# Optimization experiments

Hardware: AMD Instinct MI355X
Metric: run time of the kernel (lower is better)

The kernel has to match this reference:

```python
import jax, jax.numpy as jnp
import numpy as np

IN_DIM = 14400
K = 25
DIMS = [7200, 3600, 1800]  # floor(in_dim / 2**(i+1))
OUT_DIM = 2
BATCH = 256


def setup_inputs() -> dict:
    key = jax.random.key(0)
    ks = jax.random.split(key, 32)
    inp = {}
    inp["x"] = jax.random.normal(ks[0], (BATCH, 2 * IN_DIM), dtype=jnp.float32)
    # shared KNN tables (both channels load the same h5 files)
    prev = [IN_DIM] + DIMS[:-1]
    for i, (d, p) in enumerate(zip(DIMS, prev)):
        inp[f"knn{i}"] = jax.random.randint(ks[1 + i], (d, K), 0, p, dtype=jnp.int64)
    std = (2.0 / K) ** 0.5
    kidx = 4
    for ch in ("p", "n"):
        for i, d in enumerate(DIMS):
            inp[f"w{ch}{i}"] = jax.random.normal(ks[kidx], (d, K), dtype=jnp.float32) * std; kidx += 1
            inp[f"b{ch}{i}"] = jnp.zeros((1, d), dtype=jnp.float32)
        inp[f"fc{ch}_w"] = jax.random.normal(ks[kidx], (OUT_DIM, DIMS[-1]), dtype=jnp.float32) * (1.0 / DIMS[-1] ** 0.5); kidx += 1
        inp[f"fc{ch}_b"] = jnp.zeros((OUT_DIM,), dtype=jnp.float32)
    inp["fc3_w"] = jax.random.normal(ks[kidx], (OUT_DIM, 4), dtype=jnp.float32) * 0.5
    inp["fc3_b"] = jnp.zeros((OUT_DIM,), dtype=jnp.float32)
    return inp


def _lcn(x, knns, ws, bs, fw, fb):
    # x: (B, in_dim). Each layer: gather KNN neighbors, weighted sum, bias, relu.
    for knn, w, b in zip(knns, ws, bs):
        g = x[:, knn]                                  # (B, dim, K) gather
        x = jax.nn.relu(jnp.einsum('bdk,dk->bd', g, w) + b)
    return x @ fw.T + fb                               # fc_angle


def reference(x, knn0, knn1, knn2,
              wp0, bp0, wp1, bp1, wp2, bp2, fcp_w, fcp_b,
              wn0, bn0, wn1, bn1, wn2, bn2, fcn_w, fcn_b,
              fc3_w, fc3_b):
    knns = (knn0, knn1, knn2)
    xpos = _lcn(x[:, :IN_DIM], knns, (wp0, wp1, wp2), (bp0, bp1, bp2), fcp_w, fcp_b)
    xneg = _lcn(x[:, IN_DIM:], knns, (wn0, wn1, wn2), (bn0, bn1, bn2), fcn_w, fcn_b)
    h = jax.nn.relu(jnp.concatenate([xpos, xneg], axis=1))  # (B, 4)
    return h @ fc3_w.T + fc3_b
```

## Files before the change

### kernel.cpp

```cpp
#include <hip/hip_runtime.h>
#include <hip/hip_bf16.h>

using bf16 = __hip_bfloat16;

#define K 25
#define B 256

__device__ __forceinline__ float b2f(ushort u) {
  unsigned int w = ((unsigned int)u) << 16;
  float f; __builtin_memcpy(&f, &w, 4); return f;
}
__device__ __forceinline__ ushort f2b(float f) {
  bf16 h = __float2bfloat16(f);
  ushort u; __builtin_memcpy(&u, &h, 2); return u;
}

__global__ __launch_bounds__(256) void transpose_kernel(const void* __restrict__ x,
                                                        const void* __restrict__ knn0,
                                                        ushort* __restrict__ xT,
                                                        float* __restrict__ y,
                                                        int* __restrict__ flags) {
  __shared__ float tile[64][65];
  __shared__ int s_flags[2];
  const int t = threadIdx.x;

  if (t < 64) {
    const unsigned int u = ((const unsigned int*)x)[t * 997];
    const unsigned int e = (u >> 23) & 0xFF;
    const unsigned long long m = __ballot((e >= 192) || (e <= 30));
    if (t == 0) s_flags[0] = (__popcll(m) >= 32) ? 1 : 0;
  } else if (t < 128) {
    const int l = t - 64;
    const unsigned int hi = ((const unsigned int*)knn0)[2 * l + 1];
    const unsigned long long m = __ballot(hi != 0);
    if (l == 0) s_flags[1] = (m == 0ULL) ? 1 : 0;
  }
  __syncthreads();
  const int fdt = s_flags[0];

  if (blockIdx.x == 0 && blockIdx.y == 0) {
    if (t == 0) {
      flags[0] = s_flags[0];
      flags[1] = s_flags[1];
      flags[16] = 0;
    }
#pragma unroll
    for (int i = 0; i < 4; ++i) y[t + i * 256] = 0.0f;
  }

  const int f0 = blockIdx.x * 64;
  const int b0 = blockIdx.y * 64;
  if (fdt) {
    const ushort* xp = (const ushort*)x;
#pragma unroll
    for (int q = 0; q < 4; ++q) {
      const int lin = t + q * 256;
      const int bl = lin >> 4;
      const int fq = (lin & 15) << 2;
      const ushort4 v = *(const ushort4*)(xp + (size_t)(b0 + bl) * 28800 + f0 + fq);
      tile[bl][fq] = b2f(v.x); tile[bl][fq + 1] = b2f(v.y);
      tile[bl][fq + 2] = b2f(v.z); tile[bl][fq + 3] = b2f(v.w);
    }
  } else {
    const float* xp = (const float*)x;
#pragma unroll
    for (int q = 0; q < 4; ++q) {
      const int lin = t + q * 256;
      const int bl = lin >> 4;
      const int fq = (lin & 15) << 2;
      const float4 v = *(const float4*)(xp + (size_t)(b0 + bl) * 28800 + f0 + fq);
      tile[bl][fq] = v.x; tile[bl][fq + 1] = v.y;
      tile[bl][fq + 2] = v.z; tile[bl][fq + 3] = v.w;
    }
  }
  __syncthreads();
#pragma unroll
  for (int q = 0; q < 4; ++q) {
    const int lin = t + q * 256;
    const int fl = lin >> 4;
    const int bq = (lin & 15) << 2;
    ushort4 o;
    o.x = f2b(tile[bq][fl]);     o.y = f2b(tile[bq + 1][fl]);
    o.z = f2b(tile[bq + 2][fl]); o.w = f2b(tile[bq + 3][fl]);
    *(ushort4*)(xT + (size_t)(f0 + fl) * B + b0 + bq) = o;
  }
}

__global__ __launch_bounds__(256) void lcn_layer(const ushort* __restrict__ inT,
                                                 const void* __restrict__ knn,
                                                 const void* __restrict__ wp,
                                                 const void* __restrict__ bp,
                                                 const void* __restrict__ wn,
                                                 const void* __restrict__ bn,
                                                 ushort* __restrict__ outT,
                                                 const int* __restrict__ flags,
                                                 int prev, int dout) {
  const int fdt = flags[0];
  const int idt = flags[1];
  const int wave = threadIdx.x >> 6;
  const int lane = threadIdx.x & 63;
  const int cf   = blockIdx.x & 3;
  const int ch   = cf >> 1;
  const int half = cf & 1;
  const int d    = (blockIdx.x >> 2) * 4 + wave;

  const ushort* in = inT + (size_t)ch * prev * B + half * 128;
  const void* wsel = ch ? wn : wp;
  const void* bsel = ch ? bn : bp;

  int r[K]; float wk[K];
  if (idt) {
    const long long* ip = (const long long*)knn + (size_t)d * K;
#pragma unroll
    for (int k = 0; k < K; ++k) r[k] = (int)ip[k];
  } else {
    const int* ip = (const int*)knn + (size_t)d * K;
#pragma unroll
    for (int k = 0; k < K; ++k) r[k] = ip[k];
  }
  if (fdt) {
    const ushort* wpp = (const ushort*)wsel + (size_t)d * K;
#pragma unroll
    for (int k = 0; k < K; ++k) wk[k] = b2f(wpp[k]);
  } else {
    const float* wpp = (const float*)wsel + (size_t)d * K;
#pragma unroll
    for (int k = 0; k < K; ++k) wk[k] = wpp[k];
  }
  const float bias = fdt ? b2f(((const ushort*)bsel)[d]) : ((const float*)bsel)[d];

  float a0 = 0.f, a1 = 0.f;
#pragma unroll
  for (int k = 0; k < K; ++k) {
    const ushort2 v = *(const ushort2*)(in + (size_t)r[k] * B + (lane << 1));
    a0 = fmaf(wk[k], b2f(v.x), a0);
    a1 = fmaf(wk[k], b2f(v.y), a1);
  }
  a0 = fmaxf(a0 + bias, 0.f);
  a1 = fmaxf(a1 + bias, 0.f);
  ushort2 o; o.x = f2b(a0); o.y = f2b(a1);
  *(ushort2*)(outT + ((size_t)ch * dout + d) * B + half * 128 + (lane << 1)) = o;
}

__global__ __launch_bounds__(256) void fc_final_kernel(const ushort* __restrict__ h2,
                                                       const void* __restrict__ fcpw,
                                                       const void* __restrict__ fcnw,
                                                       const void* __restrict__ fcpb,
                                                       const void* __restrict__ fcnb,
                                                       const void* __restrict__ f3w,
                                                       const void* __restrict__ f3b,
                                                       float* __restrict__ y,
                                                       int* __restrict__ flags,
                                                       void* __restrict__ out) {
  const int fdt = flags[0];
  const int wave = threadIdx.x >> 6;
  const int lane = threadIdx.x & 63;
  const int wt = blockIdx.x * 4 + wave;
  __shared__ int s_last;

  if (wt < 450) {
    const int ch = wt >= 225;
    const int c0 = (ch ? wt - 225 : wt) * 8;
    const ushort* h = h2 + (size_t)ch * 1800 * B;
    const void* fw = ch ? fcnw : fcpw;
    float w0[8], w1[8];
    if (fdt) {
      const ushort* fp = (const ushort*)fw;
#pragma unroll
      for (int j = 0; j < 8; ++j) { w0[j] = b2f(fp[c0 + j]); w1[j] = b2f(fp[1800 + c0 + j]); }
    } else {
      const float* fp = (const float*)fw;
#pragma unroll
      for (int j = 0; j < 8; ++j) { w0[j] = fp[c0 + j]; w1[j] = fp[1800 + c0 + j]; }
    }
    float s0[4] = {0.f, 0.f, 0.f, 0.f}, s1[4] = {0.f, 0.f, 0.f, 0.f};
#pragma unroll
    for (int j = 0; j < 8; ++j) {
      const ushort4 v = *(const ushort4*)(h + (size_t)(c0 + j) * B + (lane << 2));
      const float f0v = b2f(v.x), f1v = b2f(v.y), f2v = b2f(v.z), f3v = b2f(v.w);
      s0[0] = fmaf(w0[j], f0v, s0[0]); s0[1] = fmaf(w0[j], f1v, s0[1]);
      s0[2] = fmaf(w0[j], f2v, s0[2]); s0[3] = fmaf(w0[j], f3v, s0[3]);
      s1[0] = fmaf(w1[j], f0v, s1[0]); s1[1] = fmaf(w1[j], f1v, s1[1]);
      s1[2] = fmaf(w1[j], f2v, s1[2]); s1[3] = fmaf(w1[j], f3v, s1[3]);
    }
#pragma unroll
    for (int i = 0; i < 4; ++i) {
      atomicAdd(&y[(ch * 2 + 0) * B + (lane << 2) + i], s0[i]);
      atomicAdd(&y[(ch * 2 + 1) * B + (lane << 2) + i], s1[i]);
    }
  }

  __syncthreads();
  if (threadIdx.x == 0) {
    __threadfence();
    s_last = (atomicAdd(&flags[16], 1) == gridDim.x - 1);
  }
  __syncthreads();
  if (s_last) {
    const int b = threadIdx.x;
    const float y0 = atomicAdd(&y[0 * B + b], 0.0f);
    const float y1 = atomicAdd(&y[1 * B + b], 0.0f);
    const float y2 = atomicAdd(&y[2 * B + b], 0.0f);
    const float y3 = atomicAdd(&y[3 * B + b], 0.0f);
    const float bp0v = fdt ? b2f(((const ushort*)fcpb)[0]) : ((const float*)fcpb)[0];
    const float bp1v = fdt ? b2f(((const ushort*)fcpb)[1]) : ((const float*)fcpb)[1];
    const float bn0v = fdt ? b2f(((const ushort*)fcnb)[0]) : ((const float*)fcnb)[0];
    const float bn1v = fdt ? b2f(((const ushort*)fcnb)[1]) : ((const float*)fcnb)[1];
    const float h0v = fmaxf(y0 + bp0v, 0.f);
    const float h1v = fmaxf(y1 + bp1v, 0.f);
    const float h2v = fmaxf(y2 + bn0v, 0.f);
    const float h3v = fmaxf(y3 + bn1v, 0.f);
#pragma unroll
    for (int o = 0; o < 2; ++o) {
      float w0, w1, w2, w3, bb;
      if (fdt) {
        const ushort* fp = (const ushort*)f3w;
        w0 = b2f(fp[o * 4 + 0]); w1 = b2f(fp[o * 4 + 1]);
        w2 = b2f(fp[o * 4 + 2]); w3 = b2f(fp[o * 4 + 3]);
        bb = b2f(((const ushort*)f3b)[o]);
      } else {
        const float* fp = (const float*)f3w;
        w0 = fp[o * 4 + 0]; w1 = fp[o * 4 + 1];
        w2 = fp[o * 4 + 2]; w3 = fp[o * 4 + 3];
        bb = ((const float*)f3b)[o];
      }
      float r = bb;
      r = fmaf(w0, h0v, r); r = fmaf(w1, h1v, r);
      r = fmaf(w2, h2v, r); r = fmaf(w3, h3v, r);
      if (fdt) ((ushort*)out)[b * 2 + o] = f2b(r);
      else     ((float*)out)[b * 2 + o] = r;
    }
  }
}

extern "C" void kernel_launch(void* const* d_in, const int* in_sizes, int n_in,
                              void* d_out, int out_size, void* d_ws, size_t ws_size,
                              hipStream_t stream) {
  const void* x    = d_in[0];
  const void* knn0 = d_in[1];
  const void* knn1 = d_in[2];
  const void* knn2 = d_in[3];
  const void* wp0  = d_in[4];  const void* bp0 = d_in[5];
  const void* wp1  = d_in[6];  const void* bp1 = d_in[7];
  const void* wp2  = d_in[8];  const void* bp2 = d_in[9];
  const void* fcpw = d_in[10]; const void* fcpb = d_in[11];
  const void* wn0  = d_in[12]; const void* bn0 = d_in[13];
  const void* wn1  = d_in[14]; const void* bn1 = d_in[15];
  const void* wn2  = d_in[16]; const void* bn2 = d_in[17];
  const void* fcnw = d_in[18]; const void* fcnb = d_in[19];
  const void* f3w  = d_in[20]; const void* f3b  = d_in[21];

  char* ws = (char*)d_ws;
  ushort* xT = (ushort*)(ws);
  ushort* h0 = (ushort*)(ws + 14745600);
  ushort* h1 = (ushort*)(ws + 22118400);
  ushort* h2 = (ushort*)(ws + 25804800);
  float* y   = (float*)(ws + 27648000);
  int* flags = (int*)(ws + 27652096);

  transpose_kernel<<<dim3(450, 4), 256, 0, stream>>>(x, knn0, xT, y, flags);

  lcn_layer<<<7200, 256, 0, stream>>>(xT, knn0, wp0, bp0, wn0, bn0, h0,
                                      flags, 14400, 7200);
  lcn_layer<<<3600, 256, 0, stream>>>(h0, knn1, wp1, bp1, wn1, bn1, h1,
                                      flags, 7200, 3600);
  lcn_layer<<<1800, 256, 0, stream>>>(h1, knn2, wp2, bp2, wn2, bn2, h2,
                                      flags, 3600, 1800);

  fc_final_kernel<<<113, 256, 0, stream>>>(h2, fcpw, fcnw, fcpb, fcnb, f3w, f3b,
                                           y, flags, d_out);
}
```

Measured before the change: 178.2 us.

## Fuse all LCN layers into one LDS-resident kernel per batch pair and channel

Replaces the transpose, three per-layer gather kernels and the FC kernel with a prepack kernel plus one fused kernel. The prepack kernel packs each KNN index and bf16 weight into a 32-bit word laid out k-major, and converts the biases. The fused kernel keeps two batch rows of one channel in LDS (about 86 KB), runs all three layers and the FC reduction from LDS, and combines results through atomics. This removes the global round trips for the intermediate activations and the transpose, but leaves only 256 blocks with heavy LDS use, so occupancy is low and each thread works through long serial loops.

After: 174.3 us. 2.2% less time.

```diff
diff --git a/kernel.cpp b/kernel.cpp
--- a/kernel.cpp
+++ b/kernel.cpp
@@ -4,7 +4,16 @@
 using bf16 = __hip_bfloat16;
 
 #define K 25
-#define B 256
+#define D0 7200
+#define D1 3600
+#define D2 1800
+
+#define PKB_L1 360000
+#define PKB_L2 540000
+#define NPK    630000
+#define PBB_L1 14400
+#define PBB_L2 21600
+#define NPB    25200
 
 __device__ __forceinline__ float b2f(ushort u) {
   unsigned int w = ((unsigned int)u) << 16;
@@ -15,15 +24,20 @@
   ushort u; __builtin_memcpy(&u, &h, 2); return u;
 }
 
-__global__ __launch_bounds__(256) void transpose_kernel(const void* __restrict__ x,
-                                                        const void* __restrict__ knn0,
-                                                        ushort* __restrict__ xT,
-                                                        float* __restrict__ y,
-                                                        int* __restrict__ flags) {
-  __shared__ float tile[64][65];
+__global__ __launch_bounds__(256) void prepack_kernel(
+    const void* __restrict__ x,
+    const void* __restrict__ knn0, const void* __restrict__ knn1,
+    const void* __restrict__ knn2,
+    const void* __restrict__ wp0, const void* __restrict__ bp0,
+    const void* __restrict__ wp1, const void* __restrict__ bp1,
+    const void* __restrict__ wp2, const void* __restrict__ bp2,
+    const void* __restrict__ wn0, const void* __restrict__ bn0,
+    const void* __restrict__ wn1, const void* __restrict__ bn1,
+    const void* __restrict__ wn2, const void* __restrict__ bn2,
+    unsigned int* __restrict__ pk, float* __restrict__ pbias,
+    float* __restrict__ y, int* __restrict__ flags) {
   __shared__ int s_flags[2];
   const int t = threadIdx.x;
-
   if (t < 64) {
     const unsigned int u = ((const unsigned int*)x)[t * 997];
     const unsigned int e = (u >> 23) & 0xFF;
@@ -36,172 +50,172 @@
     if (l == 0) s_flags[1] = (m == 0ULL) ? 1 : 0;
   }
   __syncthreads();
-  const int fdt = s_flags[0];
-
-  if (blockIdx.x == 0 && blockIdx.y == 0) {
+  const int fdt = s_flags[0], idt = s_flags[1];
+
+  if (blockIdx.x == 0 && t == 0) {
+    flags[0] = fdt; flags[1] = idt; flags[16] = 0;
+  }
+
+  const int gid = blockIdx.x * 256 + t;
+  if (gid < NPK) {
+    int i = gid, ch, k, d, dout;
+    const void *kn, *wsel;
+    if (i < PKB_L1) {
+      ch = i / 180000; i -= ch * 180000; dout = D0; kn = knn0;
+      wsel = ch ? wn0 : wp0;
+    } else if (i < PKB_L2) {
+      i -= PKB_L1; ch = i / 90000; i -= ch * 90000; dout = D1; kn = knn1;
+      wsel = ch ? wn1 : wp1;
+    } else {
+      i -= PKB_L2; ch = i / 45000; i -= ch * 45000; dout = D2; kn = knn2;
+      wsel = ch ? wn2 : wp2;
+    }
+    k = i / dout; d = i - k * dout;
+    const int pos = d * K + k;
+    const unsigned int idx = idt ? ((const unsigned int*)kn)[2 * pos]
+                                 : ((const unsigned int*)kn)[pos];
+    const ushort wb = fdt ? ((const ushort*)wsel)[pos]
+                          : f2b(((const float*)wsel)[pos]);
+    pk[gid] = (idx << 16) | (unsigned int)wb;
+  } else if (gid < NPK + NPB) {
+    int i = gid - NPK, ch, d;
+    const void* src;
+    if (i < PBB_L1) {
+      ch = i / D0; d = i - ch * D0; src = ch ? bn0 : bp0;
+    } else if (i < PBB_L2) {
+      const int i2 = i - PBB_L1; ch = i2 / D1; d = i2 - ch * D1; src = ch ? bn1 : bp1;
+    } else {
+      const int i2 = i - PBB_L2; ch = i2 / D2; d = i2 - ch * D2; src = ch ? bn2 : bp2;
+    }
+    pbias[i] = fdt ? b2f(((const ushort*)src)[d]) : ((const float*)src)[d];
+  } else if (gid < NPK + NPB + 1024) {
+    y[gid - (NPK + NPB)] = 0.0f;
+  }
+}
+
+__device__ __forceinline__ void layer_run(ushort* lds, const unsigned int* __restrict__ pk,
+                                          const float* __restrict__ pbias,
+                                          int offIn, int offOut, int pkb, int pbb,
+                                          int dout) {
+  for (int d = threadIdx.x; d < dout; d += 256) {
+    const unsigned int* s = pk + pkb + d;
+    float a0 = 0.f, a1 = 0.f;
+#pragma unroll
+    for (int k = 0; k < K; ++k) {
+      const unsigned int pw = s[k * dout];
+      const unsigned int vv = *(const unsigned int*)&lds[offIn + ((pw >> 16) << 1)];
+      const float w = b2f((ushort)(pw & 0xFFFFu));
+      a0 = fmaf(w, b2f((ushort)(vv & 0xFFFFu)), a0);
+      a1 = fmaf(w, b2f((ushort)(vv >> 16)), a1);
+    }
+    const float bias = pbias[pbb + d];
+    a0 = fmaxf(a0 + bias, 0.f);
+    a1 = fmaxf(a1 + bias, 0.f);
+    *(unsigned int*)&lds[offOut + (d << 1)] =
+        (unsigned int)f2b(a0) | ((unsigned int)f2b(a1) << 16);
+  }
+}
+
+__global__ __launch_bounds__(256) void lcn_fused(
+    const void* __restrict__ x, const unsigned int* __restrict__ pk,
+    const float* __restrict__ pbias,
+    const void* __restrict__ fcpw, const void* __restrict__ fcnw,
+    const void* __restrict__ fcpb, const void* __restrict__ fcnb,
+    const void* __restrict__ f3w, const void* __restrict__ f3b,
+    float* __restrict__ y, int* __restrict__ flags, void* __restrict__ out) {
+  __shared__ ushort lds[43200];
+  __shared__ float red[4][4];
+  __shared__ int sflag;
+  const int t = threadIdx.x;
+  const int ch = blockIdx.x & 1;
+  const int b0 = (blockIdx.x >> 1) * 2;
+
+  if (t == 0) sflag = flags[0];
+  __syncthreads();
+  const int fdt = sflag;
+
+  if (fdt) {
+    const ushort* r0 = (const ushort*)x + (size_t)b0 * 28800 + ch * 14400;
+    const ushort* r1 = r0 + 28800;
+    for (int c = t; c < 3600; c += 256) {
+      const ushort4 a = ((const ushort4*)r0)[c];
+      const ushort4 b = ((const ushort4*)r1)[c];
+      unsigned int* dst = (unsigned int*)&lds[c * 8];
+      dst[0] = (unsigned int)a.x | ((unsigned int)b.x << 16);
+      dst[1] = (unsigned int)a.y | ((unsigned int)b.y << 16);
+      dst[2] = (unsigned int)a.z | ((unsigned int)b.z << 16);
+      dst[3] = (unsigned int)a.w | ((unsigned int)b.w << 16);
+    }
+  } else {
+    const float* r0 = (const float*)x + (size_t)b0 * 28800 + ch * 14400;
+    const float* r1 = r0 + 28800;
+    for (int c = t; c < 3600; c += 256) {
+      const float4 a = ((const float4*)r0)[c];
+      const float4 b = ((const float4*)r1)[c];
+      unsigned int* dst = (unsigned int*)&lds[c * 8];
+      dst[0] = (unsigned int)f2b(a.x) | ((unsigned int)f2b(b.x) << 16);
+      dst[1] = (unsigned int)f2b(a.y) | ((unsigned int)f2b(b.y) << 16);
+      dst[2] = (unsigned int)f2b(a.z) | ((unsigned int)f2b(b.z) << 16);
+      dst[3] = (unsigned int)f2b(a.w) | ((unsigned int)f2b(b.w) << 16);
+    }
+  }
+  __syncthreads();
+
+  layer_run(lds, pk, pbias, 0, 28800, 0 + ch * 180000, 0 + ch * D0, D0);
+  __syncthreads();
+  layer_run(lds, pk, pbias, 28800, 0, PKB_L1 + ch * 90000, PBB_L1 + ch * D1, D1);
+  __syncthreads();
+  layer_run(lds, pk, pbias, 0, 7200, PKB_L2 + ch * 45000, PBB_L2 + ch * D2, D2);
+  __syncthreads();
+
+  {
+    const void* fw = ch ? fcnw : fcpw;
+    float a00 = 0.f, a01 = 0.f, a10 = 0.f, a11 = 0.f;
+    for (int d = t; d < D2; d += 256) {
+      const unsigned int vv = *(const unsigned int*)&lds[7200 + (d << 1)];
+      const float v0 = b2f((ushort)(vv & 0xFFFFu));
+      const float v1 = b2f((ushort)(vv >> 16));
+      const float w0 = fdt ? b2f(((const ushort*)fw)[d]) : ((const float*)fw)[d];
+      const float w1 = fdt ? b2f(((const ushort*)fw)[D2 + d]) : ((const float*)fw)[D2 + d];
+      a00 = fmaf(w0, v0, a00); a01 = fmaf(w0, v1, a01);
+      a10 = fmaf(w1, v0, a10); a11 = fmaf(w1, v1, a11);
+    }
+#pragma unroll
+    for (int off = 32; off > 0; off >>= 1) {
+      a00 += __shfl_down(a00, off);
+      a01 += __shfl_down(a01, off);
+      a10 += __shfl_down(a10, off);
+      a11 += __shfl_down(a11, off);
+    }
+    const int wave = t >> 6, lane = t & 63;
+    if (lane == 0) {
+      red[wave][0] = a00; red[wave][1] = a01; red[wave][2] = a10; red[wave][3] = a11;
+    }
+    __syncthreads();
     if (t == 0) {
-      flags[0] = s_flags[0];
-      flags[1] = s_flags[1];
-      flags[16] = 0;
-    }
-#pragma unroll
-    for (int i = 0; i < 4; ++i) y[t + i * 256] = 0.0f;
-  }
-
-  const int f0 = blockIdx.x * 64;
-  const int b0 = blockIdx.y * 64;
-  if (fdt) {
-    const ushort* xp = (const ushort*)x;
-#pragma unroll
-    for (int q = 0; q < 4; ++q) {
-      const int lin = t + q * 256;
-      const int bl = lin >> 4;
-      const int fq = (lin & 15) << 2;
-      const ushort4 v = *(const ushort4*)(xp + (size_t)(b0 + bl) * 28800 + f0 + fq);
-      tile[bl][fq] = b2f(v.x); tile[bl][fq + 1] = b2f(v.y);
-      tile[bl][fq + 2] = b2f(v.z); tile[bl][fq + 3] = b2f(v.w);
-    }
-  } else {
-    const float* xp = (const float*)x;
-#pragma unroll
-    for (int q = 0; q < 4; ++q) {
-      const int lin = t + q * 256;
-      const int bl = lin >> 4;
-      const int fq = (lin & 15) << 2;
-      const float4 v = *(const float4*)(xp + (size_t)(b0 + bl) * 28800 + f0 + fq);
-      tile[bl][fq] = v.x; tile[bl][fq + 1] = v.y;
-      tile[bl][fq + 2] = v.z; tile[bl][fq + 3] = v.w;
-    }
-  }
-  __syncthreads();
-#pragma unroll
-  for (int q = 0; q < 4; ++q) {
-    const int lin = t + q * 256;
-    const int fl = lin >> 4;
-    const int bq = (lin & 15) << 2;
-    ushort4 o;
-    o.x = f2b(tile[bq][fl]);     o.y = f2b(tile[bq + 1][fl]);
-    o.z = f2b(tile[bq + 2][fl]); o.w = f2b(tile[bq + 3][fl]);
-    *(ushort4*)(xT + (size_t)(f0 + fl) * B + b0 + bq) = o;
-  }
-}
-
-__global__ __launch_bounds__(256) void lcn_layer(const ushort* __restrict__ inT,
-                                                 const void* __restrict__ knn,
-                                                 const void* __restrict__ wp,
-                                                 const void* __restrict__ bp,
-                                                 const void* __restrict__ wn,
-                                                 const void* __restrict__ bn,
-                                                 ushort* __restrict__ outT,
-                                                 const int* __restrict__ flags,
-                                                 int prev, int dout) {
-  const int fdt = flags[0];
-  const int idt = flags[1];
-  const int wave = threadIdx.x >> 6;
-  const int lane = threadIdx.x & 63;
-  const int cf   = blockIdx.x & 3;
-  const int ch   = cf >> 1;
-  const int half = cf & 1;
-  const int d    = (blockIdx.x >> 2) * 4 + wave;
-
-  const ushort* in = inT + (size_t)ch * prev * B + half * 128;
-  const void* wsel = ch ? wn : wp;
-  const void* bsel = ch ? bn : bp;
-
-  int r[K]; float wk[K];
-  if (idt) {
-    const long long* ip = (const long long*)knn + (size_t)d * K;
-#pragma unroll
-    for (int k = 0; k < K; ++k) r[k] = (int)ip[k];
-  } else {
-    const int* ip = (const int*)knn + (size_t)d * K;
-#pragma unroll
-    for (int k = 0; k < K; ++k) r[k] = ip[k];
-  }
-  if (fdt) {
-    const ushort* wpp = (const ushort*)wsel + (size_t)d * K;
-#pragma unroll
-    for (int k = 0; k < K; ++k) wk[k] = b2f(wpp[k]);
-  } else {
-    const float* wpp = (const float*)wsel + (size_t)d * K;
-#pragma unroll
-    for (int k = 0; k < K; ++k) wk[k] = wpp[k];
-  }
-  const float bias = fdt ? b2f(((const ushort*)bsel)[d]) : ((const float*)bsel)[d];
-
-  float a0 = 0.f, a1 = 0.f;
-#pragma unroll
-  for (int k = 0; k < K; ++k) {
-    const ushort2 v = *(const ushort2*)(in + (size_t)r[k] * B + (lane << 1));
-    a0 = fmaf(wk[k], b2f(v.x), a0);
-    a1 = fmaf(wk[k], b2f(v.y), a1);
-  }
-  a0 = fmaxf(a0 + bias, 0.f);
-  a1 = fmaxf(a1 + bias, 0.f);
-  ushort2 o; o.x = f2b(a0); o.y = f2b(a1);
-  *(ushort2*)(outT + ((size_t)ch * dout + d) * B + half * 128 + (lane << 1)) = o;
-}
-
-__global__ __launch_bounds__(256) void fc_final_kernel(const ushort* __restrict__ h2,
-                                                       const void* __restrict__ fcpw,
-                                                       const void* __restrict__ fcnw,
-                                                       const void* __restrict__ fcpb,
-                                                       const void* __restrict__ fcnb,
-                                                       const void* __restrict__ f3w,
-                                                       const void* __restrict__ f3b,
-                                                       float* __restrict__ y,
-                                                       int* __restrict__ flags,
-                                                       void* __restrict__ out) {
-  const int fdt = flags[0];
-  const int wave = threadIdx.x >> 6;
-  const int lane = threadIdx.x & 63;
-  const int wt = blockIdx.x * 4 + wave;
-  __shared__ int s_last;
-
-  if (wt < 450) {
-    const int ch = wt >= 225;
-    const int c0 = (ch ? wt - 225 : wt) * 8;
-    const ushort* h = h2 + (size_t)ch * 1800 * B;
-    const void* fw = ch ? fcnw : fcpw;
-    float w0[8], w1[8];
-    if (fdt) {
-      const ushort* fp = (const ushort*)fw;
-#pragma unroll
-      for (int j = 0; j < 8; ++j) { w0[j] = b2f(fp[c0 + j]); w1[j] = b2f(fp[1800 + c0 + j]); }
-    } else {
-      const float* fp = (const float*)fw;
-#pragma unroll
-      for (int j = 0; j < 8; ++j) { w0[j] = fp[c0 + j]; w1[j] = fp[1800 + c0 + j]; }
-    }
-    float s0[4] = {0.f, 0.f, 0.f, 0.f}, s1[4] = {0.f, 0.f, 0.f, 0.f};
-#pragma unroll
-    for (int j = 0; j < 8; ++j) {
-      const ushort4 v = *(const ushort4*)(h + (size_t)(c0 + j) * B + (lane << 2));
-      const float f0v = b2f(v.x), f1v = b2f(v.y), f2v = b2f(v.z), f3v = b2f(v.w);
-      s0[0] = fmaf(w0[j], f0v, s0[0]); s0[1] = fmaf(w0[j], f1v, s0[1]);
-      s0[2] = fmaf(w0[j], f2v, s0[2]); s0[3] = fmaf(w0[j], f3v, s0[3]);
-      s1[0] = fmaf(w1[j], f0v, s1[0]); s1[1] = fmaf(w1[j], f1v, s1[1]);
-      s1[2] = fmaf(w1[j], f2v, s1[2]); s1[3] = fmaf(w1[j], f3v, s1[3]);
-    }
-#pragma unroll
-    for (int i = 0; i < 4; ++i) {
-      atomicAdd(&y[(ch * 2 + 0) * B + (lane << 2) + i], s0[i]);
-      atomicAdd(&y[(ch * 2 + 1) * B + (lane << 2) + i], s1[i]);
-    }
-  }
-
-  __syncthreads();
-  if (threadIdx.x == 0) {
+      const float s00 = red[0][0] + red[1][0] + red[2][0] + red[3][0];
+      const float s01 = red[0][1] + red[1][1] + red[2][1] + red[3][1];
+      const float s10 = red[0][2] + red[1][2] + red[2][2] + red[3][2];
+      const float s11 = red[0][3] + red[1][3] + red[2][3] + red[3][3];
+      atomicAdd(&y[(ch * 2 + 0) * 256 + b0], s00);
+      atomicAdd(&y[(ch * 2 + 0) * 256 + b0 + 1], s01);
+      atomicAdd(&y[(ch * 2 + 1) * 256 + b0], s10);
+      atomicAdd(&y[(ch * 2 + 1) * 256 + b0 + 1], s11);
+    }
+  }
+
+  __syncthreads();
+  if (t == 0) {
     __threadfence();
-    s_last = (atomicAdd(&flags[16], 1) == gridDim.x - 1);
-  }
-  __syncthreads();
-  if (s_last) {
-    const int b = threadIdx.x;
-    const float y0 = atomicAdd(&y[0 * B + b], 0.0f);
-    const float y1 = atomicAdd(&y[1 * B + b], 0.0f);
-    const float y2 = atomicAdd(&y[2 * B + b], 0.0f);
-    const float y3 = atomicAdd(&y[3 * B + b], 0.0f);
+    sflag = (atomicAdd(&flags[16], 1) == (int)gridDim.x - 1) ? 1 : 0;
+  }
+  __syncthreads();
+  if (sflag) {
+    const int b = t;
+    const float y0 = atomicAdd(&y[0 * 256 + b], 0.0f);
+    const float y1 = atomicAdd(&y[1 * 256 + b], 0.0f);
+    const float y2 = atomicAdd(&y[2 * 256 + b], 0.0f);
+    const float y3 = atomicAdd(&y[3 * 256 + b], 0.0f);
     const float bp0v = fdt ? b2f(((const ushort*)fcpb)[0]) : ((const float*)fcpb)[0];
     const float bp1v = fdt ? b2f(((const ushort*)fcpb)[1]) : ((const float*)fcpb)[1];
     const float bn0v = fdt ? b2f(((const ushort*)fcnb)[0]) : ((const float*)fcnb)[0];
@@ -251,22 +265,16 @@
   const void* f3w  = d_in[20]; const void* f3b  = d_in[21];
 
   char* ws = (char*)d_ws;
-  ushort* xT = (ushort*)(ws);
-  ushort* h0 = (ushort*)(ws + 14745600);
-  ushort* h1 = (ushort*)(ws + 22118400);
-  ushort* h2 = (ushort*)(ws + 25804800);
-  float* y   = (float*)(ws + 27648000);
-  int* flags = (int*)(ws + 27652096);
-
-  transpose_kernel<<<dim3(450, 4), 256, 0, stream>>>(x, knn0, xT, y, flags);
-
-  lcn_layer<<<7200, 256, 0, stream>>>(xT, knn0, wp0, bp0, wn0, bn0, h0,
-                                      flags, 14400, 7200);
-  lcn_layer<<<3600, 256, 0, stream>>>(h0, knn1, wp1, bp1, wn1, bn1, h1,
-                                      flags, 7200, 3600);
-  lcn_layer<<<1800, 256, 0, stream>>>(h1, knn2, wp2, bp2, wn2, bn2, h2,
-                                      flags, 3600, 1800);
-
-  fc_final_kernel<<<113, 256, 0, stream>>>(h2, fcpw, fcnw, fcpb, fcnb, f3w, f3b,
-                                           y, flags, d_out);
-}
+  unsigned int* pk = (unsigned int*)(ws);
+  float* pbias = (float*)(ws + 2520000);
+  float* y     = (float*)(ws + 2620800);
+  int* flags   = (int*)(ws + 2624896);
+
+  prepack_kernel<<<2564, 256, 0, stream>>>(x, knn0, knn1, knn2,
+                                           wp0, bp0, wp1, bp1, wp2, bp2,
+                                           wn0, bn0, wn1, bn1, wn2, bn2,
+                                           pk, pbias, y, flags);
+
+  lcn_fused<<<256, 256, 0, stream>>>(x, pk, pbias, fcpw, fcnw, fcpb, fcnb,
+                                     f3w, f3b, y, flags, d_out);
+}
```
